# Kernel tuning notes

Measured on AMD Instinct MI355X. Metric: run time of the kernel, lower is better.

The kernel has to match this reference:

```python
import jax, jax.numpy as jnp
import numpy as np

TOP_K = 2
NORM_P = 1  # moe_normalize_expert_weights


def setup_inputs() -> dict:
    key = jax.random.key(0)
    k1, k2 = jax.random.split(key)
    B, S, H, E = 4, 4096, 4096, 64
    x = jax.random.normal(k1, (B, S, H), dtype=jnp.float32)
    # Linear(H, E, bias=False) weight, torch layout [E, H]
    W = jax.random.normal(k2, (E, H), dtype=jnp.float32) * (1.0 / np.sqrt(H))
    return {"x": x, "W": W}


def reference(x, W):
    H = x.shape[-1]
    xt = x.reshape(-1, H)                      # [T, H]
    logits = jnp.einsum('th,eh->te', xt, W)    # [T, E]
    scores = jax.nn.softmax(logits, axis=-1)   # [T, E]
    expert_weights, expert_indices = jax.lax.top_k(scores, TOP_K)  # [T, K]
    # p=1 norm over the selected weights (values are positive post-softmax)
    norm = jnp.sum(jnp.abs(expert_weights), axis=-1, keepdims=True)
    expert_weights = expert_weights / norm
    return scores, expert_weights, expert_indices
```

## Files before the change

### kernel.cpp

```cpp
#include <hip/hip_runtime.h>
#include <math.h>

#define TOKS 16384
#define HD   4096
#define NE   64
#define MT   64
#define KT   64
#define NTHR 512
#define LST  72

typedef unsigned int   u32;
typedef unsigned short u16;
typedef short v8s __attribute__((ext_vector_type(8)));
typedef float v4f __attribute__((ext_vector_type(4)));

__device__ __forceinline__ void split2(float a, float b, u32& hi, u32& lo) {
    u32 ua = __float_as_uint(a), ub = __float_as_uint(b);
    hi = (ub & 0xffff0000u) | (ua >> 16);
    float la = a - __uint_as_float(ua & 0xffff0000u);
    float lb = b - __uint_as_float(ub & 0xffff0000u);
    lo = (__float_as_uint(lb) & 0xffff0000u) | (__float_as_uint(la) >> 16);
}

__global__ __launch_bounds__(256) void wsplit_kernel(const float* __restrict__ W,
                                                     u16* __restrict__ wh, u16* __restrict__ wl) {
    const int gid = blockIdx.x * 256 + threadIdx.x;
    const float4 f = ((const float4*)W)[gid];
    u32 h0, h1, l0, l1;
    split2(f.x, f.y, h0, l0);
    split2(f.z, f.w, h1, l1);
    u32* whp = (u32*)wh; u32* wlp = (u32*)wl;
    whp[gid * 2 + 0] = h0; whp[gid * 2 + 1] = h1;
    wlp[gid * 2 + 0] = l0; wlp[gid * 2 + 1] = l1;
}

__global__ __launch_bounds__(NTHR) void router_kernel(
    const float* __restrict__ x, const u16* __restrict__ wh, const u16* __restrict__ wl,
    float* __restrict__ scores, float* __restrict__ wout, float* __restrict__ iout)
{
    __shared__ u16 Xh[2][MT][LST], Xl[2][MT][LST];
    __shared__ u16 Wh[2][NE][LST], Wl[2][NE][LST];
    __shared__ float Ls[MT][NE + 1];
    __shared__ float Ssum[MT], Smax[MT];

    const int t    = threadIdx.x;
    const int tok0 = blockIdx.x * MT;
    const int srow = t >> 3;
    const int sc   = t & 7;
    const int lane = t & 63;
    const int w    = t >> 6;
    const int wt   = w & 3;
    const int we   = w >> 1 & 2 ? 0 : 0;
    const int weh  = w >> 2;
    const int q    = lane >> 4;
    const int r    = lane & 15;

    v4f acc0 = {0.f, 0.f, 0.f, 0.f};
    v4f acc1 = {0.f, 0.f, 0.f, 0.f};

    const size_t xbase = (size_t)(tok0 + srow) * HD;
    const size_t wbase = (size_t)srow * HD;

    float4 xr0, xr1; uint4 whr, wlr;

    {
        const int k0 = 0;
        xr0 = *(const float4*)&x[xbase + k0 + sc * 4];
        xr1 = *(const float4*)&x[xbase + k0 + 32 + sc * 4];
        whr = *(const uint4*)&wh[wbase + k0 + sc * 8];
        wlr = *(const uint4*)&wl[wbase + k0 + sc * 8];
    }

    const int arow  = wt * 16 + r;
    const int brow0 = weh * 32 + r;
    const int brow1 = weh * 32 + 16 + r;

    for (int tile = 0; tile < HD / KT; ++tile) {
        const int buf = tile & 1;
        {
            u32 h0, h1, l0, l1;
            split2(xr0.x, xr0.y, h0, l0);
            split2(xr0.z, xr0.w, h1, l1);
            *(u32*)&Xh[buf][srow][sc * 4]     = h0; *(u32*)&Xh[buf][srow][sc * 4 + 2] = h1;
            *(u32*)&Xl[buf][srow][sc * 4]     = l0; *(u32*)&Xl[buf][srow][sc * 4 + 2] = l1;
            split2(xr1.x, xr1.y, h0, l0);
            split2(xr1.z, xr1.w, h1, l1);
            *(u32*)&Xh[buf][srow][32 + sc * 4]     = h0; *(u32*)&Xh[buf][srow][32 + sc * 4 + 2] = h1;
            *(u32*)&Xl[buf][srow][32 + sc * 4]     = l0; *(u32*)&Xl[buf][srow][32 + sc * 4 + 2] = l1;
            *(uint4*)&Wh[buf][srow][sc * 8] = whr;
            *(uint4*)&Wl[buf][srow][sc * 8] = wlr;
        }
        if (tile + 1 < HD / KT) {
            const int k0 = (tile + 1) * KT;
            xr0 = *(const float4*)&x[xbase + k0 + sc * 4];
            xr1 = *(const float4*)&x[xbase + k0 + 32 + sc * 4];
            whr = *(const uint4*)&wh[wbase + k0 + sc * 8];
            wlr = *(const uint4*)&wl[wbase + k0 + sc * 8];
        }
        __syncthreads();
#pragma unroll
        for (int c = 0; c < 2; ++c) {
            const int ko = c * 32 + q * 8;
            v8s ah  = *(const v8s*)&Xh[buf][arow][ko];
            v8s al  = *(const v8s*)&Xl[buf][arow][ko];
            v8s bh0 = *(const v8s*)&Wh[buf][brow0][ko];
            v8s bl0 = *(const v8s*)&Wl[buf][brow0][ko];
            v8s bh1 = *(const v8s*)&Wh[buf][brow1][ko];
            v8s bl1 = *(const v8s*)&Wl[buf][brow1][ko];
            acc0 = __builtin_amdgcn_mfma_f32_16x16x32_bf16(ah, bh0, acc0, 0, 0, 0);
            acc0 = __builtin_amdgcn_mfma_f32_16x16x32_bf16(al, bh0, acc0, 0, 0, 0);
            acc0 = __builtin_amdgcn_mfma_f32_16x16x32_bf16(ah, bl0, acc0, 0, 0, 0);
            acc1 = __builtin_amdgcn_mfma_f32_16x16x32_bf16(ah, bh1, acc1, 0, 0, 0);
            acc1 = __builtin_amdgcn_mfma_f32_16x16x32_bf16(al, bh1, acc1, 0, 0, 0);
            acc1 = __builtin_amdgcn_mfma_f32_16x16x32_bf16(ah, bl1, acc1, 0, 0, 0);
        }
        __syncthreads();
    }

#pragma unroll
    for (int reg = 0; reg < 4; ++reg) {
        Ls[wt * 16 + q * 4 + reg][weh * 32 + r]      = acc0[reg];
        Ls[wt * 16 + q * 4 + reg][weh * 32 + 16 + r] = acc1[reg];
    }
    __syncthreads();

    if (t < MT) {
        const int tk = t;
        float m = -3.402823466e+38f;
        for (int e = 0; e < NE; ++e) m = fmaxf(m, Ls[tk][e]);
        float s = 0.f;
        float v1 = -1.f, v2 = -1.f;
        int   i1 = 0, i2 = 0;
        for (int e = 0; e < NE; ++e) {
            const float ex = expf(Ls[tk][e] - m);
            s += ex;
            if (ex > v1)      { v2 = v1; i2 = i1; v1 = ex; i1 = e; }
            else if (ex > v2) { v2 = ex; i2 = e; }
        }
        const float s1 = v1 / s, s2 = v2 / s;
        const float ws_ = s1 + s2;
        wout[(size_t)(tok0 + tk) * 2 + 0] = s1 / ws_;
        wout[(size_t)(tok0 + tk) * 2 + 1] = s2 / ws_;
        iout[(size_t)(tok0 + tk) * 2 + 0] = (float)i1;
        iout[(size_t)(tok0 + tk) * 2 + 1] = (float)i2;
        Ssum[tk] = s;
        Smax[tk] = m;
    }
    __syncthreads();

#pragma unroll
    for (int it = 0; it < 8; ++it) {
        const int f  = it * NTHR + t;
        const int tk = f >> 6, e = f & 63;
        scores[(size_t)(tok0 + tk) * NE + e] = expf(Ls[tk][e] - Smax[tk]) / Ssum[tk];
    }
}

extern "C" void kernel_launch(void* const* d_in, const int* in_sizes, int n_in,
                              void* d_out, int out_size, void* d_ws, size_t ws_size,
                              hipStream_t stream) {
    (void)in_sizes; (void)n_in; (void)out_size; (void)ws_size;
    const float* x = (const float*)d_in[0];
    const float* W = (const float*)d_in[1];
    float* out    = (float*)d_out;
    float* scores = out;
    float* wout   = scores + (size_t)TOKS * NE;
    float* iout   = wout   + (size_t)TOKS * 2;

    u16* wh = (u16*)d_ws;
    u16* wl = wh + (size_t)NE * HD;

    wsplit_kernel<<<dim3(256), dim3(256), 0, stream>>>(W, wh, wl);
    router_kernel<<<dim3(TOKS / MT), dim3(NTHR), 0, stream>>>(x, wh, wl, scores, wout, iout);
}
```

Measured before the change: 393.0 us.

## Halve token tile, restructure double-buffer pipeline with one barrier per K-step

Shrinks the block to 32 tokens with 256 threads, so there are twice as many blocks, and asks for two blocks per CU through launch bounds. The K loop is reordered: the next tile is loaded into registers before the MFMAs and written to the other shared buffer afterwards, leaving a single barrier per iteration so global latency overlaps compute. W is now loaded 64 rows by 4 threads each with wider vector stores. In exchange, each block reuses W across fewer tokens, which increases total W traffic, and the softmax tail uses fewer active threads per block.

```diff
diff --git a/kernel.cpp b/kernel.cpp
--- a/kernel.cpp
+++ b/kernel.cpp
@@ -1,13 +1,14 @@
 #include <hip/hip_runtime.h>
 #include <math.h>
 
-#define TOKS 16384
-#define HD   4096
-#define NE   64
-#define MT   64
-#define KT   64
-#define NTHR 512
-#define LST  72
+#define TOKS  16384
+#define HD    4096
+#define NE    64
+#define MT    32
+#define KT    64
+#define NTHR  256
+#define LST   72
+#define NTILE (HD / KT)
 
 typedef unsigned int   u32;
 typedef unsigned short u16;
@@ -34,7 +35,7 @@
     wlp[gid * 2 + 0] = l0; wlp[gid * 2 + 1] = l1;
 }
 
-__global__ __launch_bounds__(NTHR) void router_kernel(
+__global__ __launch_bounds__(NTHR, 2) void router_kernel(
     const float* __restrict__ x, const u16* __restrict__ wh, const u16* __restrict__ wl,
     float* __restrict__ scores, float* __restrict__ wout, float* __restrict__ iout)
 {
@@ -45,59 +46,60 @@
 
     const int t    = threadIdx.x;
     const int tok0 = blockIdx.x * MT;
-    const int srow = t >> 3;
-    const int sc   = t & 7;
+    const int srow = t >> 3, sc = t & 7;
+    const int wrow = t >> 2, wc = t & 3;
     const int lane = t & 63;
     const int w    = t >> 6;
-    const int wt   = w & 3;
-    const int we   = w >> 1 & 2 ? 0 : 0;
-    const int weh  = w >> 2;
-    const int q    = lane >> 4;
-    const int r    = lane & 15;
+    const int wt   = w & 1;
+    const int weh  = w >> 1;
+    const int q    = lane >> 4, r = lane & 15;
+    const int arow  = wt * 16 + r;
+    const int brow0 = weh * 32 + r;
+    const int brow1 = weh * 32 + 16 + r;
 
     v4f acc0 = {0.f, 0.f, 0.f, 0.f};
     v4f acc1 = {0.f, 0.f, 0.f, 0.f};
 
     const size_t xbase = (size_t)(tok0 + srow) * HD;
-    const size_t wbase = (size_t)srow * HD;
+    const size_t wbase = (size_t)wrow * HD;
 
-    float4 xr0, xr1; uint4 whr, wlr;
+    float4 xr0, xr1;
+    uint4  whr0, whr1, wlr0, wlr1;
 
-    {
-        const int k0 = 0;
-        xr0 = *(const float4*)&x[xbase + k0 + sc * 4];
-        xr1 = *(const float4*)&x[xbase + k0 + 32 + sc * 4];
-        whr = *(const uint4*)&wh[wbase + k0 + sc * 8];
-        wlr = *(const uint4*)&wl[wbase + k0 + sc * 8];
-    }
+#define LOAD_TILE(K0)                                               \
+    do {                                                            \
+        xr0  = *(const float4*)&x[xbase + (K0) + sc * 4];           \
+        xr1  = *(const float4*)&x[xbase + (K0) + 32 + sc * 4];      \
+        whr0 = *(const uint4*)&wh[wbase + (K0) + wc * 8];           \
+        whr1 = *(const uint4*)&wh[wbase + (K0) + 32 + wc * 8];      \
+        wlr0 = *(const uint4*)&wl[wbase + (K0) + wc * 8];           \
+        wlr1 = *(const uint4*)&wl[wbase + (K0) + 32 + wc * 8];      \
+    } while (0)
 
-    const int arow  = wt * 16 + r;
-    const int brow0 = weh * 32 + r;
-    const int brow1 = weh * 32 + 16 + r;
+#define STORE_TILE(B)                                               \
+    do {                                                            \
+        u32 h0, h1, l0, l1;                                         \
+        split2(xr0.x, xr0.y, h0, l0);                               \
+        split2(xr0.z, xr0.w, h1, l1);                               \
+        *(uint2*)&Xh[B][srow][sc * 4]      = make_uint2(h0, h1);    \
+        *(uint2*)&Xl[B][srow][sc * 4]      = make_uint2(l0, l1);    \
+        split2(xr1.x, xr1.y, h0, l0);                               \
+        split2(xr1.z, xr1.w, h1, l1);                               \
+        *(uint2*)&Xh[B][srow][32 + sc * 4] = make_uint2(h0, h1);    \
+        *(uint2*)&Xl[B][srow][32 + sc * 4] = make_uint2(l0, l1);    \
+        *(uint4*)&Wh[B][wrow][wc * 8]      = whr0;                  \
+        *(uint4*)&Wh[B][wrow][32 + wc * 8] = whr1;                  \
+        *(uint4*)&Wl[B][wrow][wc * 8]      = wlr0;                  \
+        *(uint4*)&Wl[B][wrow][32 + wc * 8] = wlr1;                  \
+    } while (0)
 
-    for (int tile = 0; tile < HD / KT; ++tile) {
+    LOAD_TILE(0);
+    STORE_TILE(0);
+    __syncthreads();
+
+    for (int tile = 0; tile < NTILE; ++tile) {
         const int buf = tile & 1;
-        {
-            u32 h0, h1, l0, l1;
-            split2(xr0.x, xr0.y, h0, l0);
-            split2(xr0.z, xr0.w, h1, l1);
-            *(u32*)&Xh[buf][srow][sc * 4]     = h0; *(u32*)&Xh[buf][srow][sc * 4 + 2] = h1;
-            *(u32*)&Xl[buf][srow][sc * 4]     = l0; *(u32*)&Xl[buf][srow][sc * 4 + 2] = l1;
-            split2(xr1.x, xr1.y, h0, l0);
-            split2(xr1.z, xr1.w, h1, l1);
-            *(u32*)&Xh[buf][srow][32 + sc * 4]     = h0; *(u32*)&Xh[buf][srow][32 + sc * 4 + 2] = h1;
-            *(u32*)&Xl[buf][srow][32 + sc * 4]     = l0; *(u32*)&Xl[buf][srow][32 + sc * 4 + 2] = l1;
-            *(uint4*)&Wh[buf][srow][sc * 8] = whr;
-            *(uint4*)&Wl[buf][srow][sc * 8] = wlr;
-        }
-        if (tile + 1 < HD / KT) {
-            const int k0 = (tile + 1) * KT;
-            xr0 = *(const float4*)&x[xbase + k0 + sc * 4];
-            xr1 = *(const float4*)&x[xbase + k0 + 32 + sc * 4];
-            whr = *(const uint4*)&wh[wbase + k0 + sc * 8];
-            wlr = *(const uint4*)&wl[wbase + k0 + sc * 8];
-        }
-        __syncthreads();
+        if (tile + 1 < NTILE) LOAD_TILE((tile + 1) * KT);
 #pragma unroll
         for (int c = 0; c < 2; ++c) {
             const int ko = c * 32 + q * 8;
@@ -114,6 +116,7 @@
             acc1 = __builtin_amdgcn_mfma_f32_16x16x32_bf16(al, bh1, acc1, 0, 0, 0);
             acc1 = __builtin_amdgcn_mfma_f32_16x16x32_bf16(ah, bl1, acc1, 0, 0, 0);
         }
+        if (tile + 1 < NTILE) STORE_TILE(buf ^ 1);
         __syncthreads();
     }
 
@@ -149,7 +152,7 @@
     __syncthreads();
 
 #pragma unroll
-    for (int it = 0; it < 8; ++it) {
+    for (int it = 0; it < (MT * NE) / NTHR; ++it) {
         const int f  = it * NTHR + t;
         const int tk = f >> 6, e = f & 63;
         scores[(size_t)(tok0 + tk) * NE + e] = expf(Ls[tk][e] - Smax[tk]) / Ssum[tk];
```

Measured after the change: 392.5 us. No clear change (-0.1%).
